# Optimization experiments

Hardware: AMD Instinct MI355X
Metric: run time of the kernel (lower is better)

Reference implementation:

```python
import jax, jax.numpy as jnp
import numpy as np

IN_CH = 512
MID = max(IN_CH // 8, 1)


def setup_inputs() -> dict:
    key = jax.random.key(0)
    ks = jax.random.split(key, 8)
    B, C, H, W = 4, IN_CH, 64, 64
    s = 0.05
    x = jax.random.normal(ks[0], (B, C, H, W), dtype=jnp.float32)
    wq = jax.random.normal(ks[1], (MID, C), dtype=jnp.float32) * s
    bq = jnp.zeros((MID,), dtype=jnp.float32)
    wk = jax.random.normal(ks[2], (MID, C), dtype=jnp.float32) * s
    bk = jnp.zeros((MID,), dtype=jnp.float32)
    wv = jax.random.normal(ks[3], (C, C), dtype=jnp.float32) * s
    bv = jnp.zeros((C,), dtype=jnp.float32)
    alpha = jnp.ones((1,), dtype=jnp.float32) * 0.5  # nonzero so attention path is exercised
    return {"x": x, "wq": wq, "bq": bq, "wk": wk, "bk": bk, "wv": wv, "bv": bv, "alpha": alpha}


def reference(x, wq, bq, wk, bk, wv, bv, alpha):
    B, C, H, W = x.shape
    N = H * W
    xf = x.reshape(B, C, N)  # [B, C, N]
    # 1x1 convs == per-position channel GEMMs
    q = jnp.einsum('mc,bcn->bnm', wq, xf) + bq  # [B, N, mid]
    k = jnp.einsum('mc,bcn->bmn', wk, xf) + bk[None, :, None]  # [B, mid, N]
    v = jnp.einsum('dc,bcn->bdn', wv, xf) + bv[None, :, None]  # [B, C, N]
    attn = jax.nn.softmax(jnp.einsum('bnm,bmk->bnk', q, k), axis=-1)  # [B, N, N]
    out = jnp.einsum('bdn,bkn->bdk', v, attn)  # v @ attn^T -> [B, C, N]
    out = out.reshape(B, C, H, W)
    return alpha * out + x
```

## Files before the change

### kernel.cpp

```cpp
#include <hip/hip_runtime.h>

#define BB 4
#define CD 512
#define NP 4096
#define MID 64
#define PSTR 88

typedef _Float16 half8 __attribute__((ext_vector_type(8)));
typedef _Float16 half4 __attribute__((ext_vector_type(4)));
typedef float floatx4 __attribute__((ext_vector_type(4)));

#define LOG2E 1.4426950408889634f

__global__ __launch_bounds__(256) void prep_w(
    const float* __restrict__ wq, const float* __restrict__ wk,
    const float* __restrict__ wv, const float* __restrict__ bq,
    const float* __restrict__ bk, const float* __restrict__ bv,
    _Float16* __restrict__ w_h, float* __restrict__ bias) {
  int idx = blockIdx.x * 256 + threadIdx.x;
  for (int i = idx; i < 640 * 512; i += gridDim.x * 256) {
    int r = i >> 9, c = i & 511;
    float v = (r < 64) ? wq[(r << 9) + c] * LOG2E
            : (r < 128) ? wk[((r - 64) << 9) + c]
                        : wv[((r - 128) << 9) + c];
    w_h[i] = (_Float16)v;
  }
  if (idx < 640) {
    float v = (idx < 64) ? bq[idx] * LOG2E
            : (idx < 128) ? bk[idx - 64]
                          : bv[idx - 128];
    bias[idx] = v;
  }
}

__global__ __launch_bounds__(256) void transpose_x(const float* __restrict__ x,
                                                   _Float16* __restrict__ xt) {
  __shared__ float tile[64][65];
  int b = blockIdx.z, c0 = blockIdx.y * 64, n0 = blockIdx.x * 64;
  int t = threadIdx.x;
  const float* xb = x + (size_t)b * CD * NP;
#pragma unroll
  for (int k = 0; k < 16; k++) {
    int cl = k * 4 + (t >> 6);
    int nl = t & 63;
    tile[cl][nl] = xb[(size_t)(c0 + cl) * NP + n0 + nl];
  }
  __syncthreads();
  _Float16* xtb = xt + ((size_t)b * NP + n0) * CD + c0;
#pragma unroll
  for (int k = 0; k < 2; k++) {
    int nl = k * 32 + (t >> 3);
    int cl = (t & 7) * 8;
    half8 pk;
#pragma unroll
    for (int i = 0; i < 8; i++) pk[i] = (_Float16)tile[cl + i][nl];
    *(half8*)(xtb + (size_t)nl * CD + cl) = pk;
  }
}

__global__ __launch_bounds__(256, 2) void proj_qkv(
    const _Float16* __restrict__ w_h, const float* __restrict__ bias,
    const _Float16* __restrict__ xt, _Float16* __restrict__ q_h,
    _Float16* __restrict__ k_h, _Float16* __restrict__ v_h) {
  __shared__ _Float16 xls[64 * 512];
  int t = threadIdx.x, w = t >> 6, lane = t & 63;
  int col = lane & 15, quad = lane >> 4;
  int rbh = blockIdx.x, nb = blockIdx.y, b = blockIdx.z;
  int n0 = nb * 64;
  const _Float16* xtb = xt + ((size_t)b * NP + n0) * CD;

#pragma unroll
  for (int j = 0; j < 16; j++) {
    int u = t + j * 256;
    int row = u >> 6, un = u & 63;
    *(half8*)(xls + row * 512 + ((un ^ (row & 7)) << 3)) =
        *(const half8*)(xtb + (size_t)row * CD + un * 8);
  }
  __syncthreads();

  int rw = rbh * 320 + w * 80;
  floatx4 acc[5][4] = {};
  for (int c = 0; c < CD; c += 32) {
    int cu = c >> 3;
    half8 a[5], bf[4];
#pragma unroll
    for (int i = 0; i < 5; i++)
      a[i] = *(const half8*)(w_h + (size_t)(rw + i * 16 + col) * CD + c + quad * 8);
#pragma unroll
    for (int j = 0; j < 4; j++) {
      int row = j * 16 + col;
      bf[j] = *(const half8*)(xls + row * 512 + (((cu + quad) ^ (row & 7)) << 3));
    }
#pragma unroll
    for (int i = 0; i < 5; i++)
#pragma unroll
      for (int j = 0; j < 4; j++)
        acc[i][j] = __builtin_amdgcn_mfma_f32_16x16x32_f16(a[i], bf[j], acc[i][j], 0, 0, 0);
  }

#pragma unroll
  for (int i = 0; i < 5; i++) {
    int r0 = rw + i * 16;
    float bi[4];
#pragma unroll
    for (int rr = 0; rr < 4; rr++) bi[rr] = bias[r0 + quad * 4 + rr];
    if (r0 < 128) {
      _Float16* dst = (r0 < 64 ? q_h + (size_t)b * NP * MID + r0
                               : k_h + (size_t)b * NP * MID + (r0 - 64));
#pragma unroll
      for (int j = 0; j < 4; j++) {
        int n = n0 + j * 16 + col;
        half4 pk;
#pragma unroll
        for (int rr = 0; rr < 4; rr++) pk[rr] = (_Float16)(acc[i][j][rr] + bi[rr]);
        *(half4*)(dst + (size_t)n * MID + quad * 4) = pk;
      }
    } else {
      int dbase = r0 - 128 + quad * 4;
#pragma unroll
      for (int j = 0; j < 4; j++) {
        int n = n0 + j * 16 + col;
#pragma unroll
        for (int rr = 0; rr < 4; rr++)
          v_h[((size_t)b * CD + dbase + rr) * NP + n] =
              (_Float16)(acc[i][j][rr] + bi[rr]);
      }
    }
  }
}

__global__ __launch_bounds__(256) void rowmax(const _Float16* __restrict__ q_h,
                                              const _Float16* __restrict__ k_h,
                                              float* __restrict__ M) {
  int qb = blockIdx.x, b = blockIdx.y;
  int t = threadIdx.x, w = t >> 6, lane = t & 63;
  int col = lane & 15, quad = lane >> 4;
  int q0 = qb * 32;
  const _Float16* qp = q_h + ((size_t)b * NP + q0) * MID;
  half8 bq[2][2];
#pragma unroll
  for (int qt = 0; qt < 2; qt++)
#pragma unroll
    for (int h = 0; h < 2; h++)
      bq[qt][h] = *(const half8*)(qp + (size_t)(qt * 16 + col) * MID + h * 32 + quad * 8);
  const _Float16* kp = k_h + ((size_t)b * NP + (size_t)w * 1024) * MID;
  float m[2] = {-1e30f, -1e30f};
#pragma unroll 4
  for (int n = 0; n < 1024; n += 16) {
    half8 ak0 = *(const half8*)(kp + (size_t)(n + col) * MID + quad * 8);
    half8 ak1 = *(const half8*)(kp + (size_t)(n + col) * MID + 32 + quad * 8);
#pragma unroll
    for (int qt = 0; qt < 2; qt++) {
      floatx4 s = {};
      s = __builtin_amdgcn_mfma_f32_16x16x32_f16(ak0, bq[qt][0], s, 0, 0, 0);
      s = __builtin_amdgcn_mfma_f32_16x16x32_f16(ak1, bq[qt][1], s, 0, 0, 0);
      m[qt] = fmaxf(m[qt], fmaxf(fmaxf(s[0], s[1]), fmaxf(s[2], s[3])));
    }
  }
  __shared__ float red[4][2][16];
#pragma unroll
  for (int qt = 0; qt < 2; qt++) {
    m[qt] = fmaxf(m[qt], __shfl_xor(m[qt], 16));
    m[qt] = fmaxf(m[qt], __shfl_xor(m[qt], 32));
  }
  if (quad == 0) {
    red[w][0][col] = m[0];
    red[w][1][col] = m[1];
  }
  __syncthreads();
  if (t < 32) {
    int qt = t >> 4, c = t & 15;
    float mm = fmaxf(fmaxf(red[0][qt][c], red[1][qt][c]),
                     fmaxf(red[2][qt][c], red[3][qt][c]));
    M[(size_t)b * NP + q0 + t] = mm;
  }
}

__global__ __launch_bounds__(256, 2) void attn_pv(
    const _Float16* __restrict__ q_h, const _Float16* __restrict__ k_h,
    const _Float16* __restrict__ v_h, const float* __restrict__ M,
    const float* __restrict__ x, const float* __restrict__ alpha_p,
    float* __restrict__ out) {
  int bid = blockIdx.x;
  int combo = bid & 7;
  int b = combo >> 1, ds = combo & 1;
  int qb = bid >> 3;
  int q0 = qb * 64, d0 = ds * 256;

  int t = threadIdx.x, w = t >> 6, lane = t & 63;
  int col = lane & 15, quad = lane >> 4;

  __shared__ _Float16 pbuf[2][64 * PSTR];
  __shared__ float lred[4][4][16];
  __shared__ float lfin[64];

  const _Float16* qp = q_h + ((size_t)b * NP + q0) * MID;
  half8 bq[4][2];
#pragma unroll
  for (int qt = 0; qt < 4; qt++)
#pragma unroll
    for (int h = 0; h < 2; h++)
      bq[qt][h] = *(const half8*)(qp + (size_t)(qt * 16 + col) * MID + h * 32 + quad * 8);
  float Mq[4];
#pragma unroll
  for (int qt = 0; qt < 4; qt++) Mq[qt] = M[(size_t)b * NP + q0 + qt * 16 + col];

  const _Float16* kp = k_h + (size_t)b * NP * MID;
  const _Float16* vp = v_h + ((size_t)(b * CD + d0) + w * 64) * NP;

  floatx4 acc[4][4] = {};
  float lp[4] = {0.f, 0.f, 0.f, 0.f};

  for (int ci = 0; ci < 64; ci++) {
    int nc = ci * 64;
    _Float16* pb = pbuf[ci & 1];

    const _Float16* kr = kp + (size_t)(nc + w * 16 + col) * MID;
    half8 ak0 = *(const half8*)(kr + quad * 8);
    half8 ak1 = *(const half8*)(kr + 32 + quad * 8);

    half8 av[2][4];
#pragma unroll
    for (int f = 0; f < 2; f++)
#pragma unroll
      for (int dt = 0; dt < 4; dt++)
        av[f][dt] = *(const half8*)(vp + (size_t)(dt * 16 + col) * NP + nc + f * 32 + quad * 8);

#pragma unroll
    for (int qt = 0; qt < 4; qt++) {
      floatx4 s = {};
      s = __builtin_amdgcn_mfma_f32_16x16x32_f16(ak0, bq[qt][0], s, 0, 0, 0);
      s = __builtin_amdgcn_mfma_f32_16x16x32_f16(ak1, bq[qt][1], s, 0, 0, 0);
      half4 pk;
#pragma unroll
      for (int r = 0; r < 4; r++) {
        float p = exp2f(s[r] - Mq[qt]);
        lp[qt] += p;
        pk[r] = (_Float16)p;
      }
      *(half4*)(pb + (qt * 16 + col) * PSTR + w * 16 + quad * 4) = pk;
    }
    __syncthreads();

#pragma unroll
    for (int f = 0; f < 2; f++) {
      half8 bp[4];
#pragma unroll
      for (int qt = 0; qt < 4; qt++)
        bp[qt] = *(const half8*)(pb + (qt * 16 + col) * PSTR + f * 32 + quad * 8);
#pragma unroll
      for (int dt = 0; dt < 4; dt++)
#pragma unroll
        for (int qt = 0; qt < 4; qt++)
          acc[dt][qt] = __builtin_amdgcn_mfma_f32_16x16x32_f16(av[f][dt], bp[qt], acc[dt][qt], 0, 0, 0);
    }
  }

#pragma unroll
  for (int qt = 0; qt < 4; qt++) {
    lp[qt] += __shfl_xor(lp[qt], 16);
    lp[qt] += __shfl_xor(lp[qt], 32);
    if (quad == 0) lred[w][qt][col] = lp[qt];
  }
  __syncthreads();
  if (t < 64) {
    int qt = t >> 4, c = t & 15;
    float l = lred[0][qt][c] + lred[1][qt][c] + lred[2][qt][c] + lred[3][qt][c];
    lfin[t] = alpha_p[0] / l;
  }
  __syncthreads();

  const float* xp = x + ((size_t)(b * CD + d0) + w * 64) * NP;
  float* op = out + ((size_t)(b * CD + d0) + w * 64) * NP;
#pragma unroll
  for (int dt = 0; dt < 4; dt++)
#pragma unroll
    for (int qt = 0; qt < 4; qt++) {
      float linv = lfin[qt * 16 + col];
#pragma unroll
      for (int r = 0; r < 4; r++) {
        size_t o = (size_t)(dt * 16 + quad * 4 + r) * NP + q0 + qt * 16 + col;
        op[o] = acc[dt][qt][r] * linv + xp[o];
      }
    }
}

extern "C" void kernel_launch(void* const* d_in, const int* in_sizes, int n_in,
                              void* d_out, int out_size, void* d_ws, size_t ws_size,
                              hipStream_t stream) {
  const float* x     = (const float*)d_in[0];
  const float* wq    = (const float*)d_in[1];
  const float* bq    = (const float*)d_in[2];
  const float* wk    = (const float*)d_in[3];
  const float* bk    = (const float*)d_in[4];
  const float* wv    = (const float*)d_in[5];
  const float* bv    = (const float*)d_in[6];
  const float* alpha = (const float*)d_in[7];
  float* out = (float*)d_out;

  char* ws = (char*)d_ws;
  _Float16* w_h  = (_Float16*)(ws);
  float*    bias = (float*)(ws + 655360);
  float*    Mbuf = (float*)(ws + 657920);
  _Float16* xt   = (_Float16*)(ws + 723456);
  _Float16* q_h  = (_Float16*)(ws + 17500672);
  _Float16* k_h  = (_Float16*)(ws + 19597824);
  _Float16* v_h  = (_Float16*)(ws + 21694976);

  prep_w<<<1280, 256, 0, stream>>>(wq, wk, wv, bq, bk, bv, w_h, bias);
  transpose_x<<<dim3(64, 8, BB), 256, 0, stream>>>(x, xt);
  proj_qkv<<<dim3(2, 64, BB), 256, 0, stream>>>(w_h, bias, xt, q_h, k_h, v_h);
  rowmax<<<dim3(128, BB), 256, 0, stream>>>(q_h, k_h, Mbuf);
  attn_pv<<<512, 256, 0, stream>>>(q_h, k_h, v_h, Mbuf, x, alpha, out);
}
```

Baseline: 309.3 us.

## Double key chunk size to 128 and prefetch next key tile into registers

Result: slower. 317.9 us (+2.8%).

```diff
diff --git a/kernel.cpp b/kernel.cpp
--- a/kernel.cpp
+++ b/kernel.cpp
@@ -4,7 +4,7 @@
 #define CD 512
 #define NP 4096
 #define MID 64
-#define PSTR 88
+#define PSTR 144
 
 typedef _Float16 half8 __attribute__((ext_vector_type(8)));
 typedef _Float16 half4 __attribute__((ext_vector_type(4)));
@@ -211,39 +211,56 @@
   floatx4 acc[4][4] = {};
   float lp[4] = {0.f, 0.f, 0.f, 0.f};
 
-  for (int ci = 0; ci < 64; ci++) {
-    int nc = ci * 64;
+  half8 ak[2][2];
+#pragma unroll
+  for (int kt = 0; kt < 2; kt++) {
+    const _Float16* kr = kp + (size_t)(w * 32 + kt * 16 + col) * MID;
+    ak[kt][0] = *(const half8*)(kr + quad * 8);
+    ak[kt][1] = *(const half8*)(kr + 32 + quad * 8);
+  }
+
+  for (int ci = 0; ci < 32; ci++) {
+    int nc = ci * 128;
     _Float16* pb = pbuf[ci & 1];
 
-    const _Float16* kr = kp + (size_t)(nc + w * 16 + col) * MID;
-    half8 ak0 = *(const half8*)(kr + quad * 8);
-    half8 ak1 = *(const half8*)(kr + 32 + quad * 8);
-
-    half8 av[2][4];
-#pragma unroll
-    for (int f = 0; f < 2; f++)
+    half8 av[4][4];
+#pragma unroll
+    for (int f = 0; f < 4; f++)
 #pragma unroll
       for (int dt = 0; dt < 4; dt++)
         av[f][dt] = *(const half8*)(vp + (size_t)(dt * 16 + col) * NP + nc + f * 32 + quad * 8);
 
-#pragma unroll
-    for (int qt = 0; qt < 4; qt++) {
-      floatx4 s = {};
-      s = __builtin_amdgcn_mfma_f32_16x16x32_f16(ak0, bq[qt][0], s, 0, 0, 0);
-      s = __builtin_amdgcn_mfma_f32_16x16x32_f16(ak1, bq[qt][1], s, 0, 0, 0);
-      half4 pk;
-#pragma unroll
-      for (int r = 0; r < 4; r++) {
-        float p = exp2f(s[r] - Mq[qt]);
-        lp[qt] += p;
-        pk[r] = (_Float16)p;
+    half8 nk[2][2];
+    {
+      int ncn = ((ci + 1) & 31) * 128;
+      const _Float16* kr0 = kp + (size_t)(ncn + w * 32 + col) * MID;
+      nk[0][0] = *(const half8*)(kr0 + quad * 8);
+      nk[0][1] = *(const half8*)(kr0 + 32 + quad * 8);
+      const _Float16* kr1 = kp + (size_t)(ncn + w * 32 + 16 + col) * MID;
+      nk[1][0] = *(const half8*)(kr1 + quad * 8);
+      nk[1][1] = *(const half8*)(kr1 + 32 + quad * 8);
+    }
+
+#pragma unroll
+    for (int kt = 0; kt < 2; kt++)
+#pragma unroll
+      for (int qt = 0; qt < 4; qt++) {
+        floatx4 s = {};
+        s = __builtin_amdgcn_mfma_f32_16x16x32_f16(ak[kt][0], bq[qt][0], s, 0, 0, 0);
+        s = __builtin_amdgcn_mfma_f32_16x16x32_f16(ak[kt][1], bq[qt][1], s, 0, 0, 0);
+        half4 pk;
+#pragma unroll
+        for (int r = 0; r < 4; r++) {
+          float p = exp2f(s[r] - Mq[qt]);
+          lp[qt] += p;
+          pk[r] = (_Float16)p;
+        }
+        *(half4*)(pb + (qt * 16 + col) * PSTR + w * 32 + kt * 16 + quad * 4) = pk;
       }
-      *(half4*)(pb + (qt * 16 + col) * PSTR + w * 16 + quad * 4) = pk;
-    }
     __syncthreads();
 
 #pragma unroll
-    for (int f = 0; f < 2; f++) {
+    for (int f = 0; f < 4; f++) {
       half8 bp[4];
 #pragma unroll
       for (int qt = 0; qt < 4; qt++)
@@ -254,6 +271,9 @@
         for (int qt = 0; qt < 4; qt++)
           acc[dt][qt] = __builtin_amdgcn_mfma_f32_16x16x32_f16(av[f][dt], bp[qt], acc[dt][qt], 0, 0, 0);
     }
+
+    ak[0][0] = nk[0][0]; ak[0][1] = nk[0][1];
+    ak[1][0] = nk[1][0]; ak[1][1] = nk[1][1];
   }
 
 #pragma unroll
```

## Retile projection, rowmax and attention kernels for more blocks and occupancy

Applied to the files above, without the earlier changes.

Result: slower. 512.3 us (+65.6%).

```diff
diff --git a/kernel.cpp b/kernel.cpp
--- a/kernel.cpp
+++ b/kernel.cpp
@@ -4,7 +4,7 @@
 #define CD 512
 #define NP 4096
 #define MID 64
-#define PSTR 88
+#define PSTR 144
 
 typedef _Float16 half8 __attribute__((ext_vector_type(8)));
 typedef _Float16 half4 __attribute__((ext_vector_type(4)));
@@ -58,73 +58,70 @@
   }
 }
 
-__global__ __launch_bounds__(256, 2) void proj_qkv(
+__global__ __launch_bounds__(256) void proj_qkv(
     const _Float16* __restrict__ w_h, const float* __restrict__ bias,
     const _Float16* __restrict__ xt, _Float16* __restrict__ q_h,
     _Float16* __restrict__ k_h, _Float16* __restrict__ v_h) {
-  __shared__ _Float16 xls[64 * 512];
+  __shared__ _Float16 st[64 * 136];
   int t = threadIdx.x, w = t >> 6, lane = t & 63;
   int col = lane & 15, quad = lane >> 4;
-  int rbh = blockIdx.x, nb = blockIdx.y, b = blockIdx.z;
-  int n0 = nb * 64;
-  const _Float16* xtb = xt + ((size_t)b * NP + n0) * CD;
-
-#pragma unroll
-  for (int j = 0; j < 16; j++) {
-    int u = t + j * 256;
-    int row = u >> 6, un = u & 63;
-    *(half8*)(xls + row * 512 + ((un ^ (row & 7)) << 3)) =
-        *(const half8*)(xtb + (size_t)row * CD + un * 8);
-  }
-  __syncthreads();
-
-  int rw = rbh * 320 + w * 80;
-  floatx4 acc[5][4] = {};
+  int rbt = blockIdx.x, nb = blockIdx.y, b = blockIdx.z;
+  int r0 = rbt * 64, n0 = nb * 128;
+  const _Float16* xtb = xt + ((size_t)b * NP + n0 + w * 32) * CD;
+
+  floatx4 acc[4][2] = {};
   for (int c = 0; c < CD; c += 32) {
-    int cu = c >> 3;
-    half8 a[5], bf[4];
-#pragma unroll
-    for (int i = 0; i < 5; i++)
-      a[i] = *(const half8*)(w_h + (size_t)(rw + i * 16 + col) * CD + c + quad * 8);
-#pragma unroll
-    for (int j = 0; j < 4; j++) {
-      int row = j * 16 + col;
-      bf[j] = *(const half8*)(xls + row * 512 + (((cu + quad) ^ (row & 7)) << 3));
-    }
-#pragma unroll
-    for (int i = 0; i < 5; i++)
-#pragma unroll
-      for (int j = 0; j < 4; j++)
+    half8 a[4], bf[2];
+#pragma unroll
+    for (int i = 0; i < 4; i++)
+      a[i] = *(const half8*)(w_h + (size_t)(r0 + i * 16 + col) * CD + c + quad * 8);
+#pragma unroll
+    for (int j = 0; j < 2; j++)
+      bf[j] = *(const half8*)(xtb + (size_t)(j * 16 + col) * CD + c + quad * 8);
+#pragma unroll
+    for (int i = 0; i < 4; i++)
+#pragma unroll
+      for (int j = 0; j < 2; j++)
         acc[i][j] = __builtin_amdgcn_mfma_f32_16x16x32_f16(a[i], bf[j], acc[i][j], 0, 0, 0);
   }
 
-#pragma unroll
-  for (int i = 0; i < 5; i++) {
-    int r0 = rw + i * 16;
-    float bi[4];
-#pragma unroll
-    for (int rr = 0; rr < 4; rr++) bi[rr] = bias[r0 + quad * 4 + rr];
-    if (r0 < 128) {
-      _Float16* dst = (r0 < 64 ? q_h + (size_t)b * NP * MID + r0
-                               : k_h + (size_t)b * NP * MID + (r0 - 64));
-#pragma unroll
-      for (int j = 0; j < 4; j++) {
-        int n = n0 + j * 16 + col;
+  if (rbt < 2) {
+    _Float16* dst = (rbt == 0 ? q_h : k_h) + (size_t)b * NP * MID;
+#pragma unroll
+    for (int i = 0; i < 4; i++) {
+      float bi[4];
+#pragma unroll
+      for (int rr = 0; rr < 4; rr++) bi[rr] = bias[r0 + i * 16 + quad * 4 + rr];
+#pragma unroll
+      for (int j = 0; j < 2; j++) {
+        int n = n0 + w * 32 + j * 16 + col;
         half4 pk;
 #pragma unroll
         for (int rr = 0; rr < 4; rr++) pk[rr] = (_Float16)(acc[i][j][rr] + bi[rr]);
-        *(half4*)(dst + (size_t)n * MID + quad * 4) = pk;
+        *(half4*)(dst + (size_t)n * MID + i * 16 + quad * 4) = pk;
       }
-    } else {
-      int dbase = r0 - 128 + quad * 4;
-#pragma unroll
-      for (int j = 0; j < 4; j++) {
-        int n = n0 + j * 16 + col;
+    }
+  } else {
+#pragma unroll
+    for (int i = 0; i < 4; i++) {
+      float bi[4];
+#pragma unroll
+      for (int rr = 0; rr < 4; rr++) bi[rr] = bias[r0 + i * 16 + quad * 4 + rr];
+#pragma unroll
+      for (int j = 0; j < 2; j++)
 #pragma unroll
         for (int rr = 0; rr < 4; rr++)
-          v_h[((size_t)b * CD + dbase + rr) * NP + n] =
+          st[(i * 16 + quad * 4 + rr) * 136 + w * 32 + j * 16 + col] =
               (_Float16)(acc[i][j][rr] + bi[rr]);
-      }
+    }
+    __syncthreads();
+    int dbase = r0 - 128;
+#pragma unroll
+    for (int it = 0; it < 4; it++) {
+      int u = t + it * 256;
+      int row = u >> 4, un = u & 15;
+      *(half8*)(v_h + ((size_t)b * CD + dbase + row) * NP + n0 + un * 8) =
+          *(const half8*)(st + row * 136 + un * 8);
     }
   }
 }
@@ -135,48 +132,33 @@
   int qb = blockIdx.x, b = blockIdx.y;
   int t = threadIdx.x, w = t >> 6, lane = t & 63;
   int col = lane & 15, quad = lane >> 4;
-  int q0 = qb * 32;
+  int q0 = qb * 16;
   const _Float16* qp = q_h + ((size_t)b * NP + q0) * MID;
-  half8 bq[2][2];
-#pragma unroll
-  for (int qt = 0; qt < 2; qt++)
-#pragma unroll
-    for (int h = 0; h < 2; h++)
-      bq[qt][h] = *(const half8*)(qp + (size_t)(qt * 16 + col) * MID + h * 32 + quad * 8);
+  half8 bq0 = *(const half8*)(qp + (size_t)col * MID + quad * 8);
+  half8 bq1 = *(const half8*)(qp + (size_t)col * MID + 32 + quad * 8);
   const _Float16* kp = k_h + ((size_t)b * NP + (size_t)w * 1024) * MID;
-  float m[2] = {-1e30f, -1e30f};
+  float m = -1e30f;
 #pragma unroll 4
   for (int n = 0; n < 1024; n += 16) {
     half8 ak0 = *(const half8*)(kp + (size_t)(n + col) * MID + quad * 8);
     half8 ak1 = *(const half8*)(kp + (size_t)(n + col) * MID + 32 + quad * 8);
-#pragma unroll
-    for (int qt = 0; qt < 2; qt++) {
-      floatx4 s = {};
-      s = __builtin_amdgcn_mfma_f32_16x16x32_f16(ak0, bq[qt][0], s, 0, 0, 0);
-      s = __builtin_amdgcn_mfma_f32_16x16x32_f16(ak1, bq[qt][1], s, 0, 0, 0);
-      m[qt] = fmaxf(m[qt], fmaxf(fmaxf(s[0], s[1]), fmaxf(s[2], s[3])));
-    }
-  }
-  __shared__ float red[4][2][16];
-#pragma unroll
-  for (int qt = 0; qt < 2; qt++) {
-    m[qt] = fmaxf(m[qt], __shfl_xor(m[qt], 16));
-    m[qt] = fmaxf(m[qt], __shfl_xor(m[qt], 32));
-  }
-  if (quad == 0) {
-    red[w][0][col] = m[0];
-    red[w][1][col] = m[1];
-  }
-  __syncthreads();
-  if (t < 32) {
-    int qt = t >> 4, c = t & 15;
-    float mm = fmaxf(fmaxf(red[0][qt][c], red[1][qt][c]),
-                     fmaxf(red[2][qt][c], red[3][qt][c]));
+    floatx4 s = {};
+    s = __builtin_amdgcn_mfma_f32_16x16x32_f16(ak0, bq0, s, 0, 0, 0);
+    s = __builtin_amdgcn_mfma_f32_16x16x32_f16(ak1, bq1, s, 0, 0, 0);
+    m = fmaxf(m, fmaxf(fmaxf(s[0], s[1]), fmaxf(s[2], s[3])));
+  }
+  m = fmaxf(m, __shfl_xor(m, 16));
+  m = fmaxf(m, __shfl_xor(m, 32));
+  __shared__ float red[4][16];
+  if (quad == 0) red[w][col] = m;
+  __syncthreads();
+  if (t < 16) {
+    float mm = fmaxf(fmaxf(red[0][t], red[1][t]), fmaxf(red[2][t], red[3][t]));
     M[(size_t)b * NP + q0 + t] = mm;
   }
 }
 
-__global__ __launch_bounds__(256, 2) void attn_pv(
+__global__ __launch_bounds__(256, 4) void attn_pv(
     const _Float16* __restrict__ q_h, const _Float16* __restrict__ k_h,
     const _Float16* __restrict__ v_h, const float* __restrict__ M,
     const float* __restrict__ x, const float* __restrict__ alpha_p,
@@ -185,85 +167,84 @@
   int combo = bid & 7;
   int b = combo >> 1, ds = combo & 1;
   int qb = bid >> 3;
-  int q0 = qb * 64, d0 = ds * 256;
+  int q0 = qb * 32, d0 = ds * 256;
 
   int t = threadIdx.x, w = t >> 6, lane = t & 63;
   int col = lane & 15, quad = lane >> 4;
 
-  __shared__ _Float16 pbuf[2][64 * PSTR];
-  __shared__ float lred[4][4][16];
-  __shared__ float lfin[64];
+  __shared__ _Float16 pbuf[2][32 * PSTR];
+  __shared__ float lred[4][2][16];
+  __shared__ float lfin[32];
 
   const _Float16* qp = q_h + ((size_t)b * NP + q0) * MID;
-  half8 bq[4][2];
-#pragma unroll
-  for (int qt = 0; qt < 4; qt++)
+  half8 bq[2][2];
+#pragma unroll
+  for (int qt = 0; qt < 2; qt++)
 #pragma unroll
     for (int h = 0; h < 2; h++)
       bq[qt][h] = *(const half8*)(qp + (size_t)(qt * 16 + col) * MID + h * 32 + quad * 8);
-  float Mq[4];
-#pragma unroll
-  for (int qt = 0; qt < 4; qt++) Mq[qt] = M[(size_t)b * NP + q0 + qt * 16 + col];
+  float Mq[2];
+#pragma unroll
+  for (int qt = 0; qt < 2; qt++) Mq[qt] = M[(size_t)b * NP + q0 + qt * 16 + col];
 
   const _Float16* kp = k_h + (size_t)b * NP * MID;
   const _Float16* vp = v_h + ((size_t)(b * CD + d0) + w * 64) * NP;
 
-  floatx4 acc[4][4] = {};
-  float lp[4] = {0.f, 0.f, 0.f, 0.f};
-
-  for (int ci = 0; ci < 64; ci++) {
-    int nc = ci * 64;
+  floatx4 acc[4][2] = {};
+  float lp[2] = {0.f, 0.f};
+
+  for (int ci = 0; ci < 32; ci++) {
+    int nc = ci * 128;
     _Float16* pb = pbuf[ci & 1];
 
-    const _Float16* kr = kp + (size_t)(nc + w * 16 + col) * MID;
-    half8 ak0 = *(const half8*)(kr + quad * 8);
-    half8 ak1 = *(const half8*)(kr + 32 + quad * 8);
-
-    half8 av[2][4];
-#pragma unroll
-    for (int f = 0; f < 2; f++)
+#pragma unroll
+    for (int kt = 0; kt < 2; kt++) {
+      const _Float16* kr = kp + (size_t)(nc + w * 32 + kt * 16 + col) * MID;
+      half8 ak0 = *(const half8*)(kr + quad * 8);
+      half8 ak1 = *(const half8*)(kr + 32 + quad * 8);
+#pragma unroll
+      for (int qt = 0; qt < 2; qt++) {
+        floatx4 s = {};
+        s = __builtin_amdgcn_mfma_f32_16x16x32_f16(ak0, bq[qt][0], s, 0, 0, 0);
+        s = __builtin_amdgcn_mfma_f32_16x16x32_f16(ak1, bq[qt][1], s, 0, 0, 0);
+        half4 pk;
+#pragma unroll
+        for (int r = 0; r < 4; r++) {
+          float p = exp2f(s[r] - Mq[qt]);
+          lp[qt] += p;
+          pk[r] = (_Float16)p;
+        }
+        *(half4*)(pb + (qt * 16 + col) * PSTR + w * 32 + kt * 16 + quad * 4) = pk;
+      }
+    }
+    __syncthreads();
+
+#pragma unroll
+    for (int f = 0; f < 4; f++) {
+      half8 av[4];
 #pragma unroll
       for (int dt = 0; dt < 4; dt++)
-        av[f][dt] = *(const half8*)(vp + (size_t)(dt * 16 + col) * NP + nc + f * 32 + quad * 8);
-
-#pragma unroll
-    for (int qt = 0; qt < 4; qt++) {
-      floatx4 s = {};
-      s = __builtin_amdgcn_mfma_f32_16x16x32_f16(ak0, bq[qt][0], s, 0, 0, 0);
-      s = __builtin_amdgcn_mfma_f32_16x16x32_f16(ak1, bq[qt][1], s, 0, 0, 0);
-      half4 pk;
-#pragma unroll
-      for (int r = 0; r < 4; r++) {
-        float p = exp2f(s[r] - Mq[qt]);
-        lp[qt] += p;
-        pk[r] = (_Float16)p;
-      }
-      *(half4*)(pb + (qt * 16 + col) * PSTR + w * 16 + quad * 4) = pk;
-    }
-    __syncthreads();
-
-#pragma unroll
-    for (int f = 0; f < 2; f++) {
-      half8 bp[4];
-#pragma unroll
-      for (int qt = 0; qt < 4; qt++)
+        av[dt] = *(const half8*)(vp + (size_t)(dt * 16 + col) * NP + nc + f * 32 + quad * 8);
+      half8 bp[2];
+#pragma unroll
+      for (int qt = 0; qt < 2; qt++)
         bp[qt] = *(const half8*)(pb + (qt * 16 + col) * PSTR + f * 32 + quad * 8);
 #pragma unroll
       for (int dt = 0; dt < 4; dt++)
 #pragma unroll
-        for (int qt = 0; qt < 4; qt++)
-          acc[dt][qt] = __builtin_amdgcn_mfma_f32_16x16x32_f16(av[f][dt], bp[qt], acc[dt][qt], 0, 0, 0);
-    }
-  }
-
-#pragma unroll
-  for (int qt = 0; qt < 4; qt++) {
+        for (int qt = 0; qt < 2; qt++)
+          acc[dt][qt] = __builtin_amdgcn_mfma_f32_16x16x32_f16(av[dt], bp[qt], acc[dt][qt], 0, 0, 0);
+    }
+  }
+
+#pragma unroll
+  for (int qt = 0; qt < 2; qt++) {
     lp[qt] += __shfl_xor(lp[qt], 16);
     lp[qt] += __shfl_xor(lp[qt], 32);
     if (quad == 0) lred[w][qt][col] = lp[qt];
   }
   __syncthreads();
-  if (t < 64) {
+  if (t < 32) {
     int qt = t >> 4, c = t & 15;
     float l = lred[0][qt][c] + lred[1][qt][c] + lred[2][qt][c] + lred[3][qt][c];
     lfin[t] = alpha_p[0] / l;
@@ -275,7 +256,7 @@
 #pragma unroll
   for (int dt = 0; dt < 4; dt++)
 #pragma unroll
-    for (int qt = 0; qt < 4; qt++) {
+    for (int qt = 0; qt < 2; qt++) {
       float linv = lfin[qt * 16 + col];
 #pragma unroll
       for (int r = 0; r < 4; r++) {
@@ -309,7 +290,7 @@
 
   prep_w<<<1280, 256, 0, stream>>>(wq, wk, wv, bq, bk, bv, w_h, bias);
   transpose_x<<<dim3(64, 8, BB), 256, 0, stream>>>(x, xt);
-  proj_qkv<<<dim3(2, 64, BB), 256, 0, stream>>>(w_h, bias, xt, q_h, k_h, v_h);
-  rowmax<<<dim3(128, BB), 256, 0, stream>>>(q_h, k_h, Mbuf);
-  attn_pv<<<512, 256, 0, stream>>>(q_h, k_h, v_h, Mbuf, x, alpha, out);
-}
+  proj_qkv<<<dim3(10, 32, BB), 256, 0, stream>>>(w_h, bias, xt, q_h, k_h, v_h);
+  rowmax<<<dim3(256, BB), 256, 0, stream>>>(q_h, k_h, Mbuf);
+  attn_pv<<<1024, 256, 0, stream>>>(q_h, k_h, v_h, Mbuf, x, alpha, out);
+}
```
